# Performance work log

Hardware: AMD Instinct MI355X
Metric: run time of the kernel (lower is better)

Reference implementation:

```python
import jax, jax.numpy as jnp
import numpy as np


def setup_inputs() -> dict:
    key = jax.random.key(0)
    kx, ky = jax.random.split(key)
    x = jax.random.normal(kx, (16, 4096, 3), dtype=jnp.float32)
    y = jax.random.normal(ky, (16, 4096, 3), dtype=jnp.float32)
    return {"x": x, "y": y}


def reference(x, y):
    # avoiding the O(b*N*M*d) difference tensor of the naive expansion.
    x2 = jnp.sum(x * x, axis=-1)                  # (b, N)
    y2 = jnp.sum(y * y, axis=-1)                  # (b, M)
    xy = jnp.einsum('bnd,bmd->bnm', x, y)         # (b, N, M)
    dist = x2[:, :, None] + y2[:, None, :] - 2.0 * xy
    min_d = jnp.min(dist, axis=2)                 # top-1 smallest over M -> (b, N)
    chamfer = jnp.sum(min_d, axis=1) / x.shape[1] # (b,)
    return jnp.sum(chamfer)
```

## Files before the change

kernel.cpp:

```cpp
#include <hip/hip_runtime.h>


constexpr int NPTS   = 4096;
constexpr int NBATCH = 16;
constexpr int BLOCK  = 256;
constexpr int XPT    = 8;
constexpr int XCHUNK = BLOCK * XPT;
constexpr int NXC    = NPTS / XCHUNK;


template <int NYC>
__global__ __launch_bounds__(BLOCK, 4) void chamfer_part_kernel(
    const float* __restrict__ x, const float* __restrict__ y,
    float* __restrict__ ws)
{
    constexpr int YTILE = NPTS / NYC;
    __shared__ float4 sy[YTILE];

    const int b      = blockIdx.x / (NXC * NYC);
    const int xchunk = (blockIdx.x / NYC) % NXC;
    const int ychunk = blockIdx.x % NYC;

    for (int i = threadIdx.x; i < YTILE; i += BLOCK) {
        const float* yp = y + ((size_t)b * NPTS + ychunk * YTILE + i) * 3;
        const float y0 = yp[0], y1 = yp[1], y2 = yp[2];
        sy[i] = make_float4(2.0f * y0, 2.0f * y1, 2.0f * y2,
                            fmaf(y2, y2, fmaf(y1, y1, y0 * y0)));
    }

    const int xbase = xchunk * XCHUNK + threadIdx.x * XPT;
    const float4* xp4 = (const float4*)(x + ((size_t)b * NPTS + xbase) * 3);
    const float4 a0 = xp4[0], a1 = xp4[1], a2 = xp4[2];
    const float4 a3 = xp4[3], a4 = xp4[4], a5 = xp4[5];
    const float xa[XPT][3] = {
        {a0.x, a0.y, a0.z}, {a0.w, a1.x, a1.y},
        {a1.z, a1.w, a2.x}, {a2.y, a2.z, a2.w},
        {a3.x, a3.y, a3.z}, {a3.w, a4.x, a4.y},
        {a4.z, a4.w, a5.x}, {a5.y, a5.z, a5.w}};

    float x2s[XPT];
    #pragma unroll
    for (int i = 0; i < XPT; ++i)
        x2s[i] = fmaf(xa[i][2], xa[i][2],
                 fmaf(xa[i][1], xa[i][1], xa[i][0] * xa[i][0]));

    __syncthreads();

    float m[XPT];
    #pragma unroll
    for (int i = 0; i < XPT; ++i) m[i] = 3.4e38f;

    #pragma unroll 2
    for (int j = 0; j < YTILE; j += 4) {
        const float4 Y0 = sy[j + 0];
        const float4 Y1 = sy[j + 1];
        const float4 Y2 = sy[j + 2];
        const float4 Y3 = sy[j + 3];
        #pragma unroll
        for (int i = 0; i < XPT; ++i) {
            const float t0 = fmaf(-xa[i][0], Y0.x,
                             fmaf(-xa[i][1], Y0.y,
                             fmaf(-xa[i][2], Y0.z, Y0.w)));
            const float t1 = fmaf(-xa[i][0], Y1.x,
                             fmaf(-xa[i][1], Y1.y,
                             fmaf(-xa[i][2], Y1.z, Y1.w)));
            const float t2 = fmaf(-xa[i][0], Y2.x,
                             fmaf(-xa[i][1], Y2.y,
                             fmaf(-xa[i][2], Y2.z, Y2.w)));
            const float t3 = fmaf(-xa[i][0], Y3.x,
                             fmaf(-xa[i][1], Y3.y,
                             fmaf(-xa[i][2], Y3.z, Y3.w)));
            m[i] = fminf(fminf(fminf(t0, t1), fminf(t2, t3)), m[i]);
        }
    }

    float* wp = ws + ((size_t)b * NYC + ychunk) * NPTS + xbase;
    const float d0 = fmaxf(x2s[0] + m[0], 0.0f);
    const float d1 = fmaxf(x2s[1] + m[1], 0.0f);
    const float d2 = fmaxf(x2s[2] + m[2], 0.0f);
    const float d3 = fmaxf(x2s[3] + m[3], 0.0f);
    const float d4 = fmaxf(x2s[4] + m[4], 0.0f);
    const float d5 = fmaxf(x2s[5] + m[5], 0.0f);
    const float d6 = fmaxf(x2s[6] + m[6], 0.0f);
    const float d7 = fmaxf(x2s[7] + m[7], 0.0f);
    ((float4*)wp)[0] = make_float4(d0, d1, d2, d3);
    ((float4*)wp)[1] = make_float4(d4, d5, d6, d7);
}


template <int NYC>
__global__ __launch_bounds__(BLOCK) void chamfer_reduce_kernel(
    const float* __restrict__ ws, float* __restrict__ out)
{
    __shared__ float swsum[BLOCK / 64];
    const int idx = blockIdx.x * BLOCK + threadIdx.x;
    const int b   = idx / NPTS;
    const int xp  = idx % NPTS;

    float mn = 3.4e38f;
    #pragma unroll
    for (int yc = 0; yc < NYC; ++yc)
        mn = fminf(mn, ws[((size_t)b * NYC + yc) * NPTS + xp]);

    float s = mn;
    for (int off = 32; off > 0; off >>= 1)
        s += __shfl_down(s, off, 64);
    const int wave = threadIdx.x >> 6;
    if ((threadIdx.x & 63) == 0) swsum[wave] = s;
    __syncthreads();
    if (threadIdx.x == 0) {
        float t = 0.f;
        #pragma unroll
        for (int w = 0; w < BLOCK / 64; ++w) t += swsum[w];
        atomicAdd(out, t * (1.0f / NPTS));
    }
}


constexpr int FB_YTILE = 256;
constexpr int FB_NYC   = NPTS / FB_YTILE;

__global__ __launch_bounds__(BLOCK) void chamfer_min_atomic_kernel(
    const float* __restrict__ x, const float* __restrict__ y,
    unsigned int* __restrict__ ws_min)
{
    __shared__ float4 sy[FB_YTILE];

    const int b      = blockIdx.x / (NXC * FB_NYC);
    const int xchunk = (blockIdx.x / FB_NYC) % NXC;
    const int ychunk = blockIdx.x % FB_NYC;

    {
        const float* yp = y + ((size_t)b * NPTS + ychunk * FB_YTILE + threadIdx.x) * 3;
        const float y0 = yp[0], y1 = yp[1], y2 = yp[2];
        sy[threadIdx.x] = make_float4(2.0f * y0, 2.0f * y1, 2.0f * y2,
                                      fmaf(y2, y2, fmaf(y1, y1, y0 * y0)));
    }

    const int xbase = xchunk * XCHUNK + threadIdx.x * XPT;
    const float4* xp4 = (const float4*)(x + ((size_t)b * NPTS + xbase) * 3);
    const float4 a0 = xp4[0], a1 = xp4[1], a2 = xp4[2];
    const float4 a3 = xp4[3], a4 = xp4[4], a5 = xp4[5];
    const float xa[XPT][3] = {
        {a0.x, a0.y, a0.z}, {a0.w, a1.x, a1.y},
        {a1.z, a1.w, a2.x}, {a2.y, a2.z, a2.w},
        {a3.x, a3.y, a3.z}, {a3.w, a4.x, a4.y},
        {a4.z, a4.w, a5.x}, {a5.y, a5.z, a5.w}};

    float x2s[XPT];
    #pragma unroll
    for (int i = 0; i < XPT; ++i)
        x2s[i] = fmaf(xa[i][2], xa[i][2],
                 fmaf(xa[i][1], xa[i][1], xa[i][0] * xa[i][0]));

    __syncthreads();

    float m[XPT];
    #pragma unroll
    for (int i = 0; i < XPT; ++i) m[i] = 3.4e38f;

    #pragma unroll 2
    for (int j = 0; j < FB_YTILE; j += 2) {
        const float4 Y0 = sy[j];
        const float4 Y1 = sy[j + 1];
        #pragma unroll
        for (int i = 0; i < XPT; ++i) {
            const float t0 = fmaf(-xa[i][0], Y0.x,
                             fmaf(-xa[i][1], Y0.y,
                             fmaf(-xa[i][2], Y0.z, Y0.w)));
            const float t1 = fmaf(-xa[i][0], Y1.x,
                             fmaf(-xa[i][1], Y1.y,
                             fmaf(-xa[i][2], Y1.z, Y1.w)));
            m[i] = fminf(m[i], fminf(t0, t1));
        }
    }

    unsigned int* wm = ws_min + (size_t)b * NPTS + xbase;
    #pragma unroll
    for (int i = 0; i < XPT; ++i) {
        const float d = fmaxf(x2s[i] + m[i], 0.0f);
        atomicMin(&wm[i], __float_as_uint(d));
    }
}

__global__ __launch_bounds__(BLOCK) void chamfer_sum_kernel(
    const unsigned int* __restrict__ ws_min, float* __restrict__ out)
{
    __shared__ float swsum[BLOCK / 64];
    const int total = NBATCH * NPTS;
    float s = 0.f;
    for (int i = blockIdx.x * BLOCK + threadIdx.x; i < total;
         i += gridDim.x * BLOCK)
        s += __uint_as_float(ws_min[i]);

    for (int off = 32; off > 0; off >>= 1)
        s += __shfl_down(s, off, 64);
    const int wave = threadIdx.x >> 6;
    if ((threadIdx.x & 63) == 0) swsum[wave] = s;
    __syncthreads();
    if (threadIdx.x == 0) {
        float t = 0.f;
        #pragma unroll
        for (int w = 0; w < BLOCK / 64; ++w) t += swsum[w];
        atomicAdd(out, t * (1.0f / NPTS));
    }
}


extern "C" void kernel_launch(void* const* d_in, const int* in_sizes, int n_in,
                              void* d_out, int out_size, void* d_ws, size_t ws_size,
                              hipStream_t stream) {
    const float* x = (const float*)d_in[0];
    const float* y = (const float*)d_in[1];
    float* out = (float*)d_out;

    hipMemsetAsync(out, 0, sizeof(float), stream);

    const size_t need32 = (size_t)NBATCH * 32 * NPTS * sizeof(float);
    const size_t need16 = (size_t)NBATCH * 16 * NPTS * sizeof(float);

    if (ws_size >= need32) {
        float* ws = (float*)d_ws;
        chamfer_part_kernel<32><<<NBATCH * NXC * 32, BLOCK, 0, stream>>>(x, y, ws);
        chamfer_reduce_kernel<32><<<NBATCH * NPTS / BLOCK, BLOCK, 0, stream>>>(ws, out);
    } else if (ws_size >= need16) {
        float* ws = (float*)d_ws;
        chamfer_part_kernel<16><<<NBATCH * NXC * 16, BLOCK, 0, stream>>>(x, y, ws);
        chamfer_reduce_kernel<16><<<NBATCH * NPTS / BLOCK, BLOCK, 0, stream>>>(ws, out);
    } else {
        unsigned int* ws_min = (unsigned int*)d_ws;
        hipMemsetAsync(ws_min, 0xFF, (size_t)NBATCH * NPTS * sizeof(unsigned int),
                       stream);
        chamfer_min_atomic_kernel<<<NBATCH * NXC * FB_NYC, BLOCK, 0, stream>>>(
            x, y, ws_min);
        chamfer_sum_kernel<<<64, BLOCK, 0, stream>>>(ws_min, out);
    }
}
```

Baseline: 85.31 us.

## Use 16 x-points per thread with 64 y-chunks and matching reduce kernel

Adds a new partial kernel in which each thread holds 16 x points in registers and each block processes a 64-point y tile over the whole batch. A 64-way min-reduce kernel is added to match. The aim is more register-level reuse of each shared-memory y load. In exchange, workspace traffic doubles, register pressure rises and may cause spills, and more workspace is required. The fallback partial kernel's inner loop is also reduced from 4 to 2 y points per iteration.

```diff
diff --git a/kernel.cpp b/kernel.cpp
--- a/kernel.cpp
+++ b/kernel.cpp
@@ -4,10 +4,109 @@
 constexpr int NPTS   = 4096;
 constexpr int NBATCH = 16;
 constexpr int BLOCK  = 256;
+
+
+constexpr int XPT16 = 16;
+constexpr int NYC64 = 64;
+constexpr int YT64  = NPTS / NYC64;
+
+__global__ __launch_bounds__(BLOCK, 4) void chamfer_part16_kernel(
+    const float* __restrict__ x, const float* __restrict__ y,
+    float* __restrict__ ws)
+{
+    __shared__ float4 sy[YT64];
+
+    const int b      = blockIdx.x / NYC64;
+    const int ychunk = blockIdx.x % NYC64;
+
+    if (threadIdx.x < YT64) {
+        const float* yp = y + ((size_t)b * NPTS + ychunk * YT64 + threadIdx.x) * 3;
+        const float y0 = yp[0], y1 = yp[1], y2 = yp[2];
+        sy[threadIdx.x] = make_float4(2.0f * y0, 2.0f * y1, 2.0f * y2,
+                                      fmaf(y2, y2, fmaf(y1, y1, y0 * y0)));
+    }
+
+    const int xbase = threadIdx.x * XPT16;
+    const float4* xp4 = (const float4*)(x + ((size_t)b * NPTS + xbase) * 3);
+    float xf[48];
+    #pragma unroll
+    for (int q = 0; q < 12; ++q) {
+        const float4 a = xp4[q];
+        xf[4 * q + 0] = a.x; xf[4 * q + 1] = a.y;
+        xf[4 * q + 2] = a.z; xf[4 * q + 3] = a.w;
+    }
+
+    __syncthreads();
+
+    float m[XPT16];
+    #pragma unroll
+    for (int i = 0; i < XPT16; ++i) m[i] = 3.4e38f;
+
+    #pragma unroll 2
+    for (int j = 0; j < YT64; j += 2) {
+        const float4 Y0 = sy[j];
+        const float4 Y1 = sy[j + 1];
+        #pragma unroll
+        for (int i = 0; i < XPT16; ++i) {
+            const float t0 = fmaf(-xf[3 * i + 0], Y0.x,
+                             fmaf(-xf[3 * i + 1], Y0.y,
+                             fmaf(-xf[3 * i + 2], Y0.z, Y0.w)));
+            const float t1 = fmaf(-xf[3 * i + 0], Y1.x,
+                             fmaf(-xf[3 * i + 1], Y1.y,
+                             fmaf(-xf[3 * i + 2], Y1.z, Y1.w)));
+            m[i] = fminf(fminf(t0, t1), m[i]);
+        }
+    }
+
+    float* wp = ws + ((size_t)b * NYC64 + ychunk) * NPTS + xbase;
+    #pragma unroll
+    for (int i = 0; i < XPT16; i += 4) {
+        float4 o;
+        float* oc = (float*)&o;
+        #pragma unroll
+        for (int k = 0; k < 4; ++k) {
+            const int p = i + k;
+            const float x2 = fmaf(xf[3 * p + 2], xf[3 * p + 2],
+                             fmaf(xf[3 * p + 1], xf[3 * p + 1],
+                                  xf[3 * p + 0] * xf[3 * p + 0]));
+            oc[k] = fmaxf(x2 + m[p], 0.0f);
+        }
+        ((float4*)wp)[i / 4] = o;
+    }
+}
+
+__global__ __launch_bounds__(BLOCK) void chamfer_reduce64_kernel(
+    const float* __restrict__ ws, float* __restrict__ out)
+{
+    __shared__ float swsum[BLOCK / 64];
+    const int idx = blockIdx.x * BLOCK + threadIdx.x;
+    const int b   = idx / NPTS;
+    const int xp  = idx % NPTS;
+
+    const float* p = ws + (size_t)b * NYC64 * NPTS + xp;
+    float mn = 3.4e38f;
+    #pragma unroll 8
+    for (int yc = 0; yc < NYC64; ++yc)
+        mn = fminf(mn, p[(size_t)yc * NPTS]);
+
+    float s = mn;
+    for (int off = 32; off > 0; off >>= 1)
+        s += __shfl_down(s, off, 64);
+    const int wave = threadIdx.x >> 6;
+    if ((threadIdx.x & 63) == 0) swsum[wave] = s;
+    __syncthreads();
+    if (threadIdx.x == 0) {
+        float t = 0.f;
+        #pragma unroll
+        for (int w = 0; w < BLOCK / 64; ++w) t += swsum[w];
+        atomicAdd(out, t * (1.0f / NPTS));
+    }
+}
+
+
 constexpr int XPT    = 8;
 constexpr int XCHUNK = BLOCK * XPT;
 constexpr int NXC    = NPTS / XCHUNK;
-
 
 template <int NYC>
 __global__ __launch_bounds__(BLOCK, 4) void chamfer_part_kernel(
@@ -51,11 +150,9 @@
     for (int i = 0; i < XPT; ++i) m[i] = 3.4e38f;
 
     #pragma unroll 2
-    for (int j = 0; j < YTILE; j += 4) {
-        const float4 Y0 = sy[j + 0];
+    for (int j = 0; j < YTILE; j += 2) {
+        const float4 Y0 = sy[j];
         const float4 Y1 = sy[j + 1];
-        const float4 Y2 = sy[j + 2];
-        const float4 Y3 = sy[j + 3];
         #pragma unroll
         for (int i = 0; i < XPT; ++i) {
             const float t0 = fmaf(-xa[i][0], Y0.x,
@@ -64,29 +161,21 @@
             const float t1 = fmaf(-xa[i][0], Y1.x,
                              fmaf(-xa[i][1], Y1.y,
                              fmaf(-xa[i][2], Y1.z, Y1.w)));
-            const float t2 = fmaf(-xa[i][0], Y2.x,
-                             fmaf(-xa[i][1], Y2.y,
-                             fmaf(-xa[i][2], Y2.z, Y2.w)));
-            const float t3 = fmaf(-xa[i][0], Y3.x,
-                             fmaf(-xa[i][1], Y3.y,
-                             fmaf(-xa[i][2], Y3.z, Y3.w)));
-            m[i] = fminf(fminf(fminf(t0, t1), fminf(t2, t3)), m[i]);
+            m[i] = fminf(fminf(t0, t1), m[i]);
         }
     }
 
     float* wp = ws + ((size_t)b * NYC + ychunk) * NPTS + xbase;
-    const float d0 = fmaxf(x2s[0] + m[0], 0.0f);
-    const float d1 = fmaxf(x2s[1] + m[1], 0.0f);
-    const float d2 = fmaxf(x2s[2] + m[2], 0.0f);
-    const float d3 = fmaxf(x2s[3] + m[3], 0.0f);
-    const float d4 = fmaxf(x2s[4] + m[4], 0.0f);
-    const float d5 = fmaxf(x2s[5] + m[5], 0.0f);
-    const float d6 = fmaxf(x2s[6] + m[6], 0.0f);
-    const float d7 = fmaxf(x2s[7] + m[7], 0.0f);
-    ((float4*)wp)[0] = make_float4(d0, d1, d2, d3);
-    ((float4*)wp)[1] = make_float4(d4, d5, d6, d7);
-}
-
+    #pragma unroll
+    for (int i = 0; i < XPT; i += 4) {
+        float4 o;
+        float* oc = (float*)&o;
+        #pragma unroll
+        for (int k = 0; k < 4; ++k)
+            oc[k] = fmaxf(x2s[i + k] + m[i + k], 0.0f);
+        ((float4*)wp)[i / 4] = o;
+    }
+}
 
 template <int NYC>
 __global__ __launch_bounds__(BLOCK) void chamfer_reduce_kernel(
@@ -117,21 +206,20 @@
 }
 
 
-constexpr int FB_YTILE = 256;
-constexpr int FB_NYC   = NPTS / FB_YTILE;
-
 __global__ __launch_bounds__(BLOCK) void chamfer_min_atomic_kernel(
     const float* __restrict__ x, const float* __restrict__ y,
     unsigned int* __restrict__ ws_min)
 {
-    __shared__ float4 sy[FB_YTILE];
-
-    const int b      = blockIdx.x / (NXC * FB_NYC);
-    const int xchunk = (blockIdx.x / FB_NYC) % NXC;
-    const int ychunk = blockIdx.x % FB_NYC;
+    constexpr int YTILE = 256;
+    constexpr int NYC   = NPTS / YTILE;
+    __shared__ float4 sy[YTILE];
+
+    const int b      = blockIdx.x / (NXC * NYC);
+    const int xchunk = (blockIdx.x / NYC) % NXC;
+    const int ychunk = blockIdx.x % NYC;
 
     {
-        const float* yp = y + ((size_t)b * NPTS + ychunk * FB_YTILE + threadIdx.x) * 3;
+        const float* yp = y + ((size_t)b * NPTS + ychunk * YTILE + threadIdx.x) * 3;
         const float y0 = yp[0], y1 = yp[1], y2 = yp[2];
         sy[threadIdx.x] = make_float4(2.0f * y0, 2.0f * y1, 2.0f * y2,
                                       fmaf(y2, y2, fmaf(y1, y1, y0 * y0)));
@@ -160,7 +248,7 @@
     for (int i = 0; i < XPT; ++i) m[i] = 3.4e38f;
 
     #pragma unroll 2
-    for (int j = 0; j < FB_YTILE; j += 2) {
+    for (int j = 0; j < YTILE; j += 2) {
         const float4 Y0 = sy[j];
         const float4 Y1 = sy[j + 1];
         #pragma unroll
@@ -216,13 +304,13 @@
 
     hipMemsetAsync(out, 0, sizeof(float), stream);
 
-    const size_t need32 = (size_t)NBATCH * 32 * NPTS * sizeof(float);
+    const size_t need64 = (size_t)NBATCH * NYC64 * NPTS * sizeof(float);
     const size_t need16 = (size_t)NBATCH * 16 * NPTS * sizeof(float);
 
-    if (ws_size >= need32) {
+    if (ws_size >= need64) {
         float* ws = (float*)d_ws;
-        chamfer_part_kernel<32><<<NBATCH * NXC * 32, BLOCK, 0, stream>>>(x, y, ws);
-        chamfer_reduce_kernel<32><<<NBATCH * NPTS / BLOCK, BLOCK, 0, stream>>>(ws, out);
+        chamfer_part16_kernel<<<NBATCH * NYC64, BLOCK, 0, stream>>>(x, y, ws);
+        chamfer_reduce64_kernel<<<NBATCH * NPTS / BLOCK, BLOCK, 0, stream>>>(ws, out);
     } else if (ws_size >= need16) {
         float* ws = (float*)d_ws;
         chamfer_part_kernel<16><<<NBATCH * NXC * 16, BLOCK, 0, stream>>>(x, y, ws);
@@ -231,7 +319,7 @@
         unsigned int* ws_min = (unsigned int*)d_ws;
         hipMemsetAsync(ws_min, 0xFF, (size_t)NBATCH * NPTS * sizeof(unsigned int),
                        stream);
-        chamfer_min_atomic_kernel<<<NBATCH * NXC * FB_NYC, BLOCK, 0, stream>>>(
+        chamfer_min_atomic_kernel<<<NBATCH * NXC * 16, BLOCK, 0, stream>>>(
             x, y, ws_min);
         chamfer_sum_kernel<<<64, BLOCK, 0, stream>>>(ws_min, out);
     }
```

Measured after the change: 95.82 us. 1.12x slower.
